# Kernel optimization log

Measured on AMD Instinct MI355X. Metric: run time of the kernel, lower is better.

Reference implementation:

```python
import jax, jax.numpy as jnp
import numpy as np

B, T, D = 8, 1024, 1024
H = 16
DH = D // H  # 64


def setup_inputs() -> dict:
    key = jax.random.key(0)
    k1, k2, k3 = jax.random.split(key, 3)
    x = jax.random.normal(k1, (B, T, D), dtype=jnp.float32)
    W_qkv = jax.random.normal(k2, (3 * D, D), dtype=jnp.float32) * (D ** -0.5)
    W_proj = jax.random.normal(k3, (D, D), dtype=jnp.float32) * (D ** -0.5)
    return {"x": x, "W_qkv": W_qkv, "W_proj": W_proj}


def reference(x, W_qkv, W_proj):
    b, t, _ = x.shape
    # qkv: [B,T,3*D] -> [B,T,3,H,DH]
    qkv = (x @ W_qkv.T).reshape(b, t, 3, H, DH)
    q, k, v = qkv[:, :, 0], qkv[:, :, 1], qkv[:, :, 2]  # [B,T,H,DH]
    scale = DH ** -0.5
    # scores: [B,H,Tq,Tk]
    scores = jnp.einsum("bqhd,bkhd->bhqk", q, k) * scale
    # NOTE: softmax over dim=-2 (the QUERY axis), as in the original module
    attn = jax.nn.softmax(scores, axis=-2)
    out = jnp.einsum("bhqk,bkhd->bqhd", attn, v).reshape(b, t, D)
    return out @ W_proj.T
```

## Files before the change

### kernel.cpp

```cpp
#include <hip/hip_runtime.h>


typedef __bf16 bf16_t;
typedef __bf16 bf16x8 __attribute__((ext_vector_type(8)));
typedef __bf16 bf16x4 __attribute__((ext_vector_type(4)));
typedef float f32x4 __attribute__((ext_vector_type(4)));
typedef unsigned short u16x8 __attribute__((ext_vector_type(8)));

#define DEV __device__ __forceinline__
#define C2 0.18033688f

DEV void gld_lds16(const bf16_t* g, bf16_t* l) {
  __builtin_amdgcn_global_load_lds(
      (const __attribute__((address_space(1))) unsigned int*)g,
      (__attribute__((address_space(3))) unsigned int*)l, 16, 0, 0);
}

DEV float exp2c(float x) { return __builtin_amdgcn_exp2f(fminf(x, 30.f)); }
DEV float sanit(float v) { return (v == v) ? fminf(fmaxf(v, -1e4f), 1e4f) : 0.f; }

DEV int sw64(int r, int kc) { return r * 64 + (((kc ^ (r + (r >> 3))) & 7) << 3); }
DEV int sw32(int r, int kc) { return r * 32 + (((kc ^ r ^ (r >> 2)) & 3) << 3); }

DEV f32x4 mfma16(bf16x8 a, bf16x8 b, f32x4 c) {
  return __builtin_amdgcn_mfma_f32_16x16x32_bf16(a, b, c, 0, 0, 0);
}

__global__ void detect_dtype(const unsigned short* x, int* flag) {
  __shared__ int smax;
  if (threadIdx.x == 0) smax = 0;
  __syncthreads();
  int m = 0;
  for (int i = threadIdx.x; i < 16384; i += 256) {
    int e = (x[i] >> 7) & 0xFF;
    m = m > e ? m : e;
  }
  atomicMax(&smax, m);
  __syncthreads();
  if (threadIdx.x == 0) *flag = (smax >= 160) ? 1 : 0;
}

__global__ void convert_in(const void* __restrict__ x, const void* __restrict__ wq,
                           const void* __restrict__ wp, bf16_t* __restrict__ xb,
                           bf16_t* __restrict__ wqb, bf16_t* __restrict__ wpb,
                           const int* __restrict__ flag) {
  int i = blockIdx.x * 256 + threadIdx.x;
  const void* src;
  bf16_t* dst;
  int off;
  if (i < 1048576) { src = x; dst = xb; off = i; }
  else if (i < 1441792) { src = wq; dst = wqb; off = i - 1048576; }
  else { src = wp; dst = wpb; off = i - 1441792; }
  if (*flag) {
    const float4* s = (const float4*)src;
    float4 a = s[off * 2], b = s[off * 2 + 1];
    bf16x8 o;
    o[0] = (bf16_t)a.x; o[1] = (bf16_t)a.y; o[2] = (bf16_t)a.z; o[3] = (bf16_t)a.w;
    o[4] = (bf16_t)b.x; o[5] = (bf16_t)b.y; o[6] = (bf16_t)b.z; o[7] = (bf16_t)b.w;
    *(bf16x8*)(dst + (size_t)off * 8) = o;
  } else {
    ((u16x8*)dst)[off] = ((const u16x8*)src)[off];
  }
}

__global__ __launch_bounds__(256, 2)
void gemm_bt(const bf16_t* __restrict__ A, int lda, const bf16_t* __restrict__ B,
             bf16_t* __restrict__ Cb, float* __restrict__ Cf, int ldc,
             int K, const int* __restrict__ f32flag) {
  __shared__ bf16_t sA[128 * 32];
  __shared__ bf16_t sB[128 * 32];
  const int tid = threadIdx.x;
  const int wave = tid >> 6, lane = tid & 63;
  const int l = lane & 15, quad = lane >> 4;
  const int row0 = blockIdx.y * 128, col0 = blockIdx.x * 128;
  const int wm = (wave >> 1) * 64, wn = (wave & 1) * 64;
  f32x4 acc[4][4];
#pragma unroll
  for (int i = 0; i < 4; ++i)
#pragma unroll
    for (int j = 0; j < 4; ++j) acc[i][j] = f32x4{0.f, 0.f, 0.f, 0.f};

  for (int k0 = 0; k0 < K; k0 += 32) {
    __syncthreads();
#pragma unroll
    for (int t = 0; t < 2; ++t) {
      int base = t * 256 + wave * 64;
      int n = base + lane;
      int r = n >> 2;
      int kc = ((n & 3) ^ r ^ (r >> 2)) & 3;
      gld_lds16(A + (size_t)(row0 + r) * lda + k0 + kc * 8, sA + base * 8);
      gld_lds16(B + (size_t)(col0 + r) * K + k0 + kc * 8, sB + base * 8);
    }
    __syncthreads();
    bf16x8 af[4], bfr[4];
#pragma unroll
    for (int i = 0; i < 4; ++i)
      af[i] = *(const bf16x8*)&sA[sw32(wm + i * 16 + l, quad)];
#pragma unroll
    for (int j = 0; j < 4; ++j)
      bfr[j] = *(const bf16x8*)&sB[sw32(wn + j * 16 + l, quad)];
#pragma unroll
    for (int i = 0; i < 4; ++i)
#pragma unroll
      for (int j = 0; j < 4; ++j)
        acc[i][j] = mfma16(af[i], bfr[j], acc[i][j]);
  }
  const bool of32 = (f32flag != nullptr) && (*f32flag != 0);
#pragma unroll
  for (int i = 0; i < 4; ++i) {
    int rr = row0 + wm + i * 16 + quad * 4;
#pragma unroll
    for (int j = 0; j < 4; ++j) {
      int cc = col0 + wn + j * 16 + l;
#pragma unroll
      for (int t = 0; t < 4; ++t) {
        float v = sanit(acc[i][j][t]);
        size_t idx = (size_t)(rr + t) * ldc + cc;
        if (of32) Cf[idx] = v; else Cb[idx] = (bf16_t)v;
      }
    }
  }
}

__global__ __launch_bounds__(256, 4)
void attn_stats(const bf16_t* __restrict__ qkv, bf16_t* __restrict__ Vts) {
  __shared__ bf16_t sK[128 * 64];
  __shared__ bf16_t sV[128 * 64];
  __shared__ float sL[128];
  const int bh = blockIdx.x, kt = blockIdx.y;
  const int b = bh >> 4, h = bh & 15;
  const int tid = threadIdx.x, wave = tid >> 6, lane = tid & 63;
  const int l = lane & 15, quad = lane >> 4;
  const size_t rowK = (size_t)b * 1024 + kt * 128;

#pragma unroll
  for (int t = 0; t < 4; ++t) {
    int base = wave * 256 + t * 64;
    int n = base + lane;
    int r = n >> 3;
    int kc = ((n & 7) ^ (r + (r >> 3))) & 7;
    gld_lds16(qkv + (rowK + r) * 3072 + 2048 + h * 64 + kc * 8, sV + base * 8);
    gld_lds16(qkv + (rowK + r) * 3072 + 1024 + h * 64 + kc * 8, sK + base * 8);
  }
  if (tid < 128) sL[tid] = 0.f;
  __syncthreads();

  float accj[8];
#pragma unroll
  for (int j = 0; j < 8; ++j) accj[j] = 0.f;

  for (int qt = 0; qt < 8; ++qt) {
    bf16x8 aq[2][2];
#pragma unroll
    for (int i = 0; i < 2; ++i)
#pragma unroll
      for (int ks = 0; ks < 2; ++ks)
        aq[i][ks] = *(const bf16x8*)&qkv[((size_t)b * 1024 + qt * 128 + wave * 32 +
                                          i * 16 + l) * 3072 + h * 64 +
                                         (ks * 4 + quad) * 8];
#pragma unroll
    for (int j = 0; j < 8; ++j) {
      f32x4 s0 = {0.f, 0.f, 0.f, 0.f}, s1 = {0.f, 0.f, 0.f, 0.f};
#pragma unroll
      for (int ks = 0; ks < 2; ++ks) {
        bf16x8 bk = *(const bf16x8*)&sK[sw64(j * 16 + l, ks * 4 + quad)];
        s0 = mfma16(aq[0][ks], bk, s0);
        s1 = mfma16(aq[1][ks], bk, s1);
      }
#pragma unroll
      for (int t = 0; t < 4; ++t)
        accj[j] += exp2c(s0[t] * C2) + exp2c(s1[t] * C2);
    }
  }
#pragma unroll
  for (int j = 0; j < 8; ++j) {
    float v = accj[j];
    v += __shfl_xor(v, 16);
    v += __shfl_xor(v, 32);
    if (lane < 16) atomicAdd(&sL[j * 16 + l], v);
  }
  __syncthreads();
  if (tid < 128) sL[tid] = 1.0f / fmaxf(sL[tid], 1e-20f);
  __syncthreads();

#pragma unroll
  for (int t = 0; t < 4; ++t) {
    int u = t * 256 + tid;
    int d = u >> 4, k0 = (u & 15) * 8;
    bf16x8 pk;
#pragma unroll
    for (int i = 0; i < 8; ++i) {
      int k = k0 + i;
      float v = (float)sV[sw64(k, d >> 3) + (d & 7)];
      pk[i] = (bf16_t)(v * sL[k]);
    }
    *(bf16x8*)&Vts[((size_t)bh * 64 + d) * 1024 + kt * 128 + k0] = pk;
  }
}

__global__ __launch_bounds__(256, 4)
void attn_out_k(const bf16_t* __restrict__ qkv, const bf16_t* __restrict__ Vts,
                bf16_t* __restrict__ attn) {
  __shared__ bf16_t sK[2][128 * 64];
  __shared__ bf16_t sT[4][16 * 40];
  const int bh = blockIdx.x, qt = blockIdx.y;
  const int b = bh >> 4, h = bh & 15;
  const int tid = threadIdx.x, wave = tid >> 6, lane = tid & 63;
  const int l = lane & 15, quad = lane >> 4;
  const bf16_t* qbase = qkv + (size_t)b * 3145728 + h * 64;

  bf16x8 bq[2][2];
#pragma unroll
  for (int i = 0; i < 2; ++i)
#pragma unroll
    for (int ks = 0; ks < 2; ++ks)
      bq[i][ks] = *(const bf16x8*)&qbase[(size_t)(qt * 128 + wave * 32 + i * 16 + l) *
                                             3072 + ks * 32 + quad * 8];
  f32x4 o[2][4];
#pragma unroll
  for (int i = 0; i < 2; ++i)
#pragma unroll
    for (int jd = 0; jd < 4; ++jd) o[i][jd] = f32x4{0.f, 0.f, 0.f, 0.f};

#pragma unroll
  for (int t = 0; t < 4; ++t) {
    int base = wave * 256 + t * 64;
    int n = base + lane;
    int r = n >> 3;
    int kc = ((n & 7) ^ (r + (r >> 3))) & 7;
    gld_lds16(qkv + ((size_t)b * 1024 + r) * 3072 + 1024 + h * 64 + kc * 8,
              sK[0] + base * 8);
  }
  bf16_t* sTw = sT[wave];

  for (int kt = 0; kt < 8; ++kt) {
    const int buf = kt & 1;
    __syncthreads();
    if (kt < 7) {
#pragma unroll
      for (int t = 0; t < 4; ++t) {
        int base = wave * 256 + t * 64;
        int n = base + lane;
        int r = n >> 3;
        int kc = ((n & 7) ^ (r + (r >> 3))) & 7;
        gld_lds16(qkv + ((size_t)b * 1024 + (kt + 1) * 128 + r) * 3072 + 1024 +
                      h * 64 + kc * 8,
                  sK[buf ^ 1] + base * 8);
      }
    }
    const bf16_t* sKb = sK[buf];

#pragma unroll
    for (int ch = 0; ch < 4; ++ch) {
      bf16x8 av[4];
#pragma unroll
      for (int jd = 0; jd < 4; ++jd)
        av[jd] = *(const bf16x8*)&Vts[((size_t)bh * 64 + jd * 16 + l) * 1024 +
                                      kt * 128 + ch * 32 + quad * 8];
#pragma unroll
      for (int i = 0; i < 2; ++i) {
        f32x4 st[2];
#pragma unroll
        for (int kk = 0; kk < 2; ++kk) {
          st[kk] = f32x4{0.f, 0.f, 0.f, 0.f};
#pragma unroll
          for (int ks = 0; ks < 2; ++ks) {
            bf16x8 ak = *(const bf16x8*)&sKb[sw64(ch * 32 + kk * 16 + l,
                                                  ks * 4 + quad)];
            st[kk] = mfma16(ak, bq[i][ks], st[kk]);
          }
        }
#pragma unroll
        for (int kk = 0; kk < 2; ++kk) {
          bf16x4 pk;
#pragma unroll
          for (int t = 0; t < 4; ++t) pk[t] = (bf16_t)exp2c(st[kk][t] * C2);
          *(bf16x4*)&sTw[l * 40 + kk * 16 + quad * 4] = pk;
        }
        bf16x8 bp = *(const bf16x8*)&sTw[l * 40 + quad * 8];
#pragma unroll
        for (int jd = 0; jd < 4; ++jd)
          o[i][jd] = mfma16(av[jd], bp, o[i][jd]);
      }
    }
  }
#pragma unroll
  for (int i = 0; i < 2; ++i) {
    size_t row = (size_t)b * 1024 + qt * 128 + wave * 32 + i * 16 + l;
#pragma unroll
    for (int jd = 0; jd < 4; ++jd) {
      bf16x4 pk;
#pragma unroll
      for (int t = 0; t < 4; ++t) pk[t] = (bf16_t)sanit(o[i][jd][t]);
      *(bf16x4*)&attn[row * 3072 + h * 64 + jd * 16 + quad * 4] = pk;
    }
  }
}

extern "C" void kernel_launch(void* const* d_in, const int* in_sizes, int n_in,
                              void* d_out, int out_size, void* d_ws, size_t ws_size,
                              hipStream_t stream) {
  (void)in_sizes; (void)n_in; (void)out_size; (void)ws_size;
  char* w = (char*)d_ws;
  bf16_t* qkv = (bf16_t*)w;
  bf16_t* xb = (bf16_t*)(w + 50331648);
  bf16_t* Vts = xb;
  bf16_t* Wqkvb = (bf16_t*)(w + 67108864);
  bf16_t* Wprojb = (bf16_t*)(w + 73400320);
  int* flag = (int*)(w + 75497472);
  bf16_t* attn = qkv + 2048;

  detect_dtype<<<1, 256, 0, stream>>>((const unsigned short*)d_in[0], flag);
  convert_in<<<6144, 256, 0, stream>>>(d_in[0], d_in[1], d_in[2],
                                       xb, Wqkvb, Wprojb, flag);

  gemm_bt<<<dim3(24, 64), 256, 0, stream>>>(xb, 1024, Wqkvb, qkv, nullptr, 3072,
                                            1024, nullptr);
  attn_stats<<<dim3(128, 8), 256, 0, stream>>>(qkv, Vts);
  attn_out_k<<<dim3(128, 8), 256, 0, stream>>>(qkv, Vts, attn);
  gemm_bt<<<dim3(8, 64), 256, 0, stream>>>(attn, 3072, Wprojb, (bf16_t*)d_out,
                                           (float*)d_out, 1024, 1024, flag);
}
```

Measured before the change: 316.5 us.

## Double-buffer GEMM LDS tiles and transpose MFMA operands for vectorized stores

The GEMM kernel now keeps two LDS buffers and issues the global-to-LDS loads for the next K slice before computing the current one, dropping one barrier per iteration so load latency can overlap with MFMA work. MFMA operands are swapped so each lane holds four consecutive columns of the output. The epilogue can then write float4 or bf16x4 vectors instead of scalar stores. Occupancy hint raised to 3 blocks per CU; doubled LDS per block and register pressure may limit that.

```diff
diff --git a/kernel.cpp b/kernel.cpp
--- a/kernel.cpp
+++ b/kernel.cpp
@@ -63,12 +63,12 @@
   }
 }
 
-__global__ __launch_bounds__(256, 2)
+__global__ __launch_bounds__(256, 3)
 void gemm_bt(const bf16_t* __restrict__ A, int lda, const bf16_t* __restrict__ B,
              bf16_t* __restrict__ Cb, float* __restrict__ Cf, int ldc,
              int K, const int* __restrict__ f32flag) {
-  __shared__ bf16_t sA[128 * 32];
-  __shared__ bf16_t sB[128 * 32];
+  __shared__ bf16_t sA[2][128 * 32];
+  __shared__ bf16_t sB[2][128 * 32];
   const int tid = threadIdx.x;
   const int wave = tid >> 6, lane = tid & 63;
   const int l = lane & 15, quad = lane >> 4;
@@ -76,47 +76,65 @@
   const int wm = (wave >> 1) * 64, wn = (wave & 1) * 64;
   f32x4 acc[4][4];
 #pragma unroll
-  for (int i = 0; i < 4; ++i)
-#pragma unroll
-    for (int j = 0; j < 4; ++j) acc[i][j] = f32x4{0.f, 0.f, 0.f, 0.f};
-
-  for (int k0 = 0; k0 < K; k0 += 32) {
+  for (int j = 0; j < 4; ++j)
+#pragma unroll
+    for (int i = 0; i < 4; ++i) acc[j][i] = f32x4{0.f, 0.f, 0.f, 0.f};
+
+#pragma unroll
+  for (int t = 0; t < 2; ++t) {
+    int base = t * 256 + wave * 64;
+    int n = base + lane;
+    int r = n >> 2;
+    int kc = ((n & 3) ^ r ^ (r >> 2)) & 3;
+    gld_lds16(A + (size_t)(row0 + r) * lda + kc * 8, sA[0] + base * 8);
+    gld_lds16(B + (size_t)(col0 + r) * K + kc * 8, sB[0] + base * 8);
+  }
+  const int iters = K >> 5;
+  for (int it = 0; it < iters; ++it) {
+    const int buf = it & 1;
     __syncthreads();
-#pragma unroll
-    for (int t = 0; t < 2; ++t) {
-      int base = t * 256 + wave * 64;
-      int n = base + lane;
-      int r = n >> 2;
-      int kc = ((n & 3) ^ r ^ (r >> 2)) & 3;
-      gld_lds16(A + (size_t)(row0 + r) * lda + k0 + kc * 8, sA + base * 8);
-      gld_lds16(B + (size_t)(col0 + r) * K + k0 + kc * 8, sB + base * 8);
-    }
-    __syncthreads();
+    if (it + 1 < iters) {
+      int k0 = (it + 1) << 5;
+#pragma unroll
+      for (int t = 0; t < 2; ++t) {
+        int base = t * 256 + wave * 64;
+        int n = base + lane;
+        int r = n >> 2;
+        int kc = ((n & 3) ^ r ^ (r >> 2)) & 3;
+        gld_lds16(A + (size_t)(row0 + r) * lda + k0 + kc * 8, sA[buf ^ 1] + base * 8);
+        gld_lds16(B + (size_t)(col0 + r) * K + k0 + kc * 8, sB[buf ^ 1] + base * 8);
+      }
+    }
     bf16x8 af[4], bfr[4];
 #pragma unroll
     for (int i = 0; i < 4; ++i)
-      af[i] = *(const bf16x8*)&sA[sw32(wm + i * 16 + l, quad)];
+      af[i] = *(const bf16x8*)&sA[buf][sw32(wm + i * 16 + l, quad)];
 #pragma unroll
     for (int j = 0; j < 4; ++j)
-      bfr[j] = *(const bf16x8*)&sB[sw32(wn + j * 16 + l, quad)];
-#pragma unroll
-    for (int i = 0; i < 4; ++i)
-#pragma unroll
-      for (int j = 0; j < 4; ++j)
-        acc[i][j] = mfma16(af[i], bfr[j], acc[i][j]);
+      bfr[j] = *(const bf16x8*)&sB[buf][sw32(wn + j * 16 + l, quad)];
+#pragma unroll
+    for (int j = 0; j < 4; ++j)
+#pragma unroll
+      for (int i = 0; i < 4; ++i)
+        acc[j][i] = mfma16(bfr[j], af[i], acc[j][i]);
   }
   const bool of32 = (f32flag != nullptr) && (*f32flag != 0);
 #pragma unroll
   for (int i = 0; i < 4; ++i) {
-    int rr = row0 + wm + i * 16 + quad * 4;
+    size_t row = row0 + wm + i * 16 + l;
 #pragma unroll
     for (int j = 0; j < 4; ++j) {
-      int cc = col0 + wn + j * 16 + l;
-#pragma unroll
-      for (int t = 0; t < 4; ++t) {
-        float v = sanit(acc[i][j][t]);
-        size_t idx = (size_t)(rr + t) * ldc + cc;
-        if (of32) Cf[idx] = v; else Cb[idx] = (bf16_t)v;
+      size_t cc = col0 + wn + j * 16 + quad * 4;
+      if (of32) {
+        float4 pk;
+        pk.x = sanit(acc[j][i][0]); pk.y = sanit(acc[j][i][1]);
+        pk.z = sanit(acc[j][i][2]); pk.w = sanit(acc[j][i][3]);
+        *(float4*)&Cf[row * ldc + cc] = pk;
+      } else {
+        bf16x4 pk;
+#pragma unroll
+        for (int t = 0; t < 4; ++t) pk[t] = (bf16_t)sanit(acc[j][i][t]);
+        *(bf16x4*)&Cb[row * ldc + cc] = pk;
       }
     }
   }
```

Result: no change. 318.2 us (+0.5%).
